# Optimization experiments

Hardware: AMD Instinct MI355X
Metric: run time of the kernel (lower is better)

The kernel has to match this reference:

```python
import jax, jax.numpy as jnp
import numpy as np

EPS = 1e-5
SLOPE = 0.2


def _ico_conv(x, neigh, w, b):
    # x: (B, C, N); neigh: (N, 7) -> gather 1-ring, flatten channel-major, linear
    g = x[:, :, neigh]                          # (B, C, N, 7)
    B, C, N, K = g.shape
    g = g.transpose(0, 2, 1, 3).reshape(B, N, C * K)
    y = jnp.einsum('bnf,of->bno', g, w) + b     # (B, N, out)
    return y.transpose(0, 2, 1)                 # (B, out, N)


def _bn(x, gamma, beta):
    # BatchNorm1d with track_running_stats=False: batch stats over (B, N)
    mean = x.mean(axis=(0, 2), keepdims=True)
    var = x.var(axis=(0, 2), keepdims=True)
    xhat = (x - mean) * jax.lax.rsqrt(var + EPS)
    return xhat * gamma[None, :, None] + beta[None, :, None]


def _lrelu(x):
    return jnp.where(x >= 0, x, SLOPE * x)


def setup_inputs() -> dict:
    key = jax.random.key(0)
    ks = jax.random.split(key, 10)
    B, IN_CH, OUT_CH = 2, 128, 64
    N_DOWN, N_UP, K = 40962, 163842, 7
    inp = {
        'x1': jax.random.normal(ks[0], (B, IN_CH, N_DOWN), jnp.float32),
        'x2': jax.random.normal(ks[1], (B, OUT_CH, N_UP), jnp.float32),
        'up_fc_w': jax.random.normal(ks[2], (OUT_CH, IN_CH), jnp.float32) * 0.05,
        'up_fc_b': jax.random.normal(ks[3], (OUT_CH,), jnp.float32) * 0.05,
        'conv1_w': jax.random.normal(ks[4], (OUT_CH, K * IN_CH), jnp.float32) * 0.05,
        'conv1_b': jax.random.normal(ks[5], (OUT_CH,), jnp.float32) * 0.05,
        'bn1_g': jnp.ones((OUT_CH,), jnp.float32),
        'bn1_b': jnp.zeros((OUT_CH,), jnp.float32),
        'conv2_w': jax.random.normal(ks[6], (OUT_CH, K * OUT_CH), jnp.float32) * 0.05,
        'conv2_b': jax.random.normal(ks[7], (OUT_CH,), jnp.float32) * 0.05,
        'bn2_g': jnp.ones((OUT_CH,), jnp.float32),
        'bn2_b': jnp.zeros((OUT_CH,), jnp.float32),
        'up_neigh': jax.random.randint(ks[8], (N_UP, 2), 0, N_DOWN, jnp.int32),
        'conv_neigh': jax.random.randint(ks[9], (N_UP, K), 0, N_UP, jnp.int32),
        'max_pool_indices': jnp.zeros((1,), jnp.int32),  # unused for up_mode='interp'
    }
    return inp


def reference(x1, x2, up_fc_w, up_fc_b, conv1_w, conv1_b, bn1_g, bn1_b,
              conv2_w, conv2_b, bn2_g, bn2_b, up_neigh, conv_neigh,
              max_pool_indices):
    # --- IcoUpSampleLayer ('interp'): Linear(in->out) then 2-neighbor mean ---
    h = jnp.einsum('bcn,oc->bno', x1, up_fc_w) + up_fc_b   # (B, N_down, out)
    h = h[:, up_neigh].mean(axis=2)                        # (B, N_up, out)
    x1_up = h.transpose(0, 2, 1)                           # (B, out, N_up)
    # --- concat skip along channels ---
    x = jnp.concatenate([x1_up, x2], axis=1)               # (B, in_ch, N_up)
    # --- (conv => BN => LeakyReLU) * 2 ---
    x = _lrelu(_bn(_ico_conv(x, conv_neigh, conv1_w, conv1_b), bn1_g, bn1_b))
    x = _lrelu(_bn(_ico_conv(x, conv_neigh, conv2_w, conv2_b), bn2_g, bn2_b))
    return x
```

## Files before the change

### kernel.cpp

```cpp
#include <hip/hip_runtime.h>
#include <hip/hip_bf16.h>

typedef __hip_bfloat16 bf16;
typedef short bf16x8 __attribute__((ext_vector_type(8)));
typedef float f32x4 __attribute__((ext_vector_type(4)));

#define ND     40962
#define NUP    163842
#define NBATCH 2
#define NTC    2561
#define NT64   2561
#define BN_EPS 1e-5
#define SLOPE  0.2f

#define OFF_W1P   0ull
#define OFF_W2P   114688ull
#define OFF_STATS 172032ull
#define OFF_H     173056ull
#define OFF_P2    (OFF_H + 2622464ull)
#define OFF_XCAT  10659328ull
#define OFF_Y     94546432ull

__device__ __forceinline__ void gload_lds16(const void* g, void* l) {
  __builtin_amdgcn_global_load_lds(
      (const __attribute__((address_space(1))) void*)g,
      (__attribute__((address_space(3))) void*)l, 16, 0, 0);
}

__device__ __forceinline__ float lrelu(float v) { return v >= 0.0f ? v : SLOPE * v; }

__global__ __launch_bounds__(256) void k_permw(const float* __restrict__ w1,
                                               const float* __restrict__ w2,
                                               bf16* __restrict__ w1p, bf16* __restrict__ w2p) {
  int t = blockIdx.x * 256 + threadIdx.x;
  if (t < 64 * 896) {
    int o = t / 896, f = t % 896;
    int kk = f / 128, c = f % 128;
    w1p[t] = __float2bfloat16(w1[o * 896 + c * 7 + kk]);
  } else if (t < 64 * 896 + 64 * 448) {
    int idx = t - 64 * 896;
    int o = idx / 448, f = idx % 448;
    int kk = f / 64, c = f % 64;
    w2p[idx] = __float2bfloat16(w2[o * 448 + c * 7 + kk]);
  }
}

__global__ __launch_bounds__(256) void k_h(const float* __restrict__ x1,
                                           const float* __restrict__ wfc,
                                           const float* __restrict__ bfc,
                                           bf16* __restrict__ h) {
  __shared__ float wl[128 * 64];
  __shared__ float bl[64];
  int tid = threadIdx.x, b = blockIdx.y;
  for (int i = tid; i < 8192; i += 256) { int o = i >> 7, c = i & 127; wl[c * 64 + o] = wfc[i]; }
  if (tid < 64) bl[tid] = bfc[tid];
  __syncthreads();
  int n = blockIdx.x * 256 + tid;
  int nc = n < ND ? n : ND - 1;
  float acc[64];
#pragma unroll
  for (int o = 0; o < 64; ++o) acc[o] = bl[o];
#pragma unroll 4
  for (int c = 0; c < 128; ++c) {
    float xv = x1[((size_t)b * 128 + c) * (size_t)ND + nc];
    const f32x4* wrow = (const f32x4*)(wl + c * 64);
#pragma unroll
    for (int og = 0; og < 16; ++og) {
      f32x4 wv = wrow[og];
      acc[og * 4 + 0] = fmaf(xv, wv[0], acc[og * 4 + 0]);
      acc[og * 4 + 1] = fmaf(xv, wv[1], acc[og * 4 + 1]);
      acc[og * 4 + 2] = fmaf(xv, wv[2], acc[og * 4 + 2]);
      acc[og * 4 + 3] = fmaf(xv, wv[3], acc[og * 4 + 3]);
    }
  }
  if (n < ND) {
    bf16* hp = h + ((size_t)b * ND + n) * 64;
#pragma unroll
    for (int og = 0; og < 8; ++og) {
      union { bf16x8 v; bf16 e[8]; } u;
#pragma unroll
      for (int j = 0; j < 8; ++j) u.e[j] = __float2bfloat16(acc[og * 8 + j]);
      ((bf16x8*)hp)[og] = u.v;
    }
  }
}

__global__ __launch_bounds__(256) void k_xcat(const float* __restrict__ x2,
                                              const bf16* __restrict__ h,
                                              const int* __restrict__ upn,
                                              bf16* __restrict__ xcat) {
  __shared__ float tt[64][65];
  __shared__ int un[64][2];
  int tid = threadIdx.x, b = blockIdx.y;
  int m0 = blockIdx.x * 64;
#pragma unroll
  for (int i = 0; i < 16; ++i) {
    int c = i * 4 + (tid >> 6);
    int ml = tid & 63;
    int m = m0 + ml; if (m >= NUP) m = NUP - 1;
    tt[c][ml] = x2[((size_t)b * 64 + c) * (size_t)NUP + m];
  }
  if (tid < 128) {
    int ml = tid >> 1, w = tid & 1;
    int m = m0 + ml; if (m >= NUP) m = NUP - 1;
    un[ml][w] = upn[(size_t)m * 2 + w];
  }
  __syncthreads();
  int ln = tid >> 2, p = tid & 3;
  int m = m0 + ln;
  if (m >= NUP) return;
  bf16* dst = xcat + ((size_t)b * NUP + m) * 128;
  if (p < 2) {
    int c0 = p * 32;
    const bf16* h0 = h + ((size_t)b * ND + un[ln][0]) * 64 + c0;
    const bf16* h1 = h + ((size_t)b * ND + un[ln][1]) * 64 + c0;
#pragma unroll
    for (int q = 0; q < 4; ++q) {
      union { bf16x8 v; bf16 e[8]; } a, bb, o_;
      a.v = ((const bf16x8*)h0)[q];
      bb.v = ((const bf16x8*)h1)[q];
#pragma unroll
      for (int j = 0; j < 8; ++j)
        o_.e[j] = __float2bfloat16(0.5f * (__bfloat162float(a.e[j]) + __bfloat162float(bb.e[j])));
      ((bf16x8*)(dst + c0))[q] = o_.v;
    }
  } else {
    int c0 = (p - 2) * 32;
#pragma unroll
    for (int q = 0; q < 4; ++q) {
      union { bf16x8 v; bf16 e[8]; } o_;
#pragma unroll
      for (int j = 0; j < 8; ++j) o_.e[j] = __float2bfloat16(tt[c0 + q * 8 + j][ln]);
      ((bf16x8*)(dst + 64 + c0))[q] = o_.v;
    }
  }
}

template <int CIN>
__global__ __launch_bounds__(256, 8) void k_conv(const bf16* __restrict__ x,
                                                 const int* __restrict__ neigh,
                                                 const bf16* __restrict__ wp,
                                                 const float* __restrict__ bias,
                                                 bf16* __restrict__ y,
                                                 float* __restrict__ partials) {
  constexpr int KS    = CIN / 32;
  constexpr int NSTEP = 7 * KS;

  __shared__ bf16 lA[2][2048];
  __shared__ bf16 lW[2][2048];
  __shared__ int nbl[448];

  int tid = threadIdx.x, b = blockIdx.y;
  int n0 = blockIdx.x * 64;
  int wv = tid >> 6, lane = tid & 63;
  int l15 = lane & 15, l4 = lane >> 4;

  for (int j = tid; j < 448; j += 256) {
    int gi = n0 * 7 + j;
    int gmax = NUP * 7 - 1;
    nbl[j] = neigh[gi <= gmax ? gi : gmax];
  }

  f32x4 acc[4];
#pragma unroll
  for (int ot = 0; ot < 4; ++ot) {
    float bv = bias[ot * 16 + l15];
    acc[ot] = (f32x4){bv, bv, bv, bv};
  }

  const bf16* xb = x + (size_t)b * NUP * CIN;
  const int srow = wv * 16 + (lane >> 2);
  const int sg   = ((lane & 3) ^ ((srow >> 1) & 3)) * 8;
  const bf16* wrow_ = wp + (size_t)srow * (7 * CIN) + sg;

  auto STAGE = [&](int buf, int t) {
    int kk = t / KS, ks = t % KS;
    int node = nbl[srow * 7 + kk];
    gload_lds16(xb + (size_t)node * CIN + ks * 32 + sg, &lA[buf][wv * 512]);
    gload_lds16(wrow_ + kk * CIN + ks * 32, &lW[buf][wv * 512]);
  };

  const int r  = wv * 16 + l15;
  const int oa = r * 32 + ((l4 ^ ((l15 >> 1) & 3)) * 8);

  __syncthreads();
  STAGE(0, 0);
  __syncthreads();

  int buf = 0;
#pragma unroll
  for (int t = 0; t < NSTEP; ++t) {
    if (t + 1 < NSTEP) STAGE(buf ^ 1, t + 1);
    bf16x8 a = *(const bf16x8*)(&lA[buf][oa]);
#pragma unroll
    for (int ot = 0; ot < 4; ++ot) {
      int o = ot * 16 + l15;
      bf16x8 bb = *(const bf16x8*)(&lW[buf][o * 32 + ((l4 ^ ((l15 >> 1) & 3)) * 8)]);
      acc[ot] = __builtin_amdgcn_mfma_f32_16x16x32_bf16(a, bb, acc[ot], 0, 0, 0);
    }
    __syncthreads();
    buf ^= 1;
  }

  float* lred = (float*)&lA[0][0];
  float s[4], q[4];
#pragma unroll
  for (int ot = 0; ot < 4; ++ot) { s[ot] = 0.0f; q[ot] = 0.0f; }
  bf16* yb = y + (size_t)b * NUP * 64;
  int nodebase = n0 + wv * 16 + l4 * 4;
#pragma unroll
  for (int i = 0; i < 4; ++i) {
    int node = nodebase + i;
    bool ok = node < NUP;
#pragma unroll
    for (int ot = 0; ot < 4; ++ot) {
      float v = acc[ot][i];
      if (ok) {
        yb[(size_t)node * 64 + ot * 16 + l15] = __float2bfloat16(v);
        s[ot] += v; q[ot] += v * v;
      }
    }
  }
#pragma unroll
  for (int ot = 0; ot < 4; ++ot) {
    s[ot] += __shfl_xor(s[ot], 16); s[ot] += __shfl_xor(s[ot], 32);
    q[ot] += __shfl_xor(q[ot], 16); q[ot] += __shfl_xor(q[ot], 32);
  }
  if (lane < 16) {
#pragma unroll
    for (int ot = 0; ot < 4; ++ot) {
      lred[(wv * 2 + 0) * 64 + ot * 16 + lane] = s[ot];
      lred[(wv * 2 + 1) * 64 + ot * 16 + lane] = q[ot];
    }
  }
  __syncthreads();
  if (tid < 128) {
    int which = tid >> 6, c = tid & 63;
    float p = lred[(0 * 2 + which) * 64 + c] + lred[(1 * 2 + which) * 64 + c] +
              lred[(2 * 2 + which) * 64 + c] + lred[(3 * 2 + which) * 64 + c];
    partials[((size_t)b * gridDim.x + blockIdx.x) * 128 + which * 64 + c] = p;
  }
}

__global__ __launch_bounds__(256) void k_red1(const float* __restrict__ p, int nblk,
                                              float* __restrict__ p2) {
  int g = blockIdx.x * 2 + threadIdx.x / 128;
  int j = threadIdx.x & 127;
  float a = 0.0f;
  for (int r = g; r < nblk; r += 128) a += p[(size_t)r * 128 + j];
  p2[(size_t)g * 128 + j] = a;
}

__global__ __launch_bounds__(128) void k_stats(const float* __restrict__ p2,
                                               const float* __restrict__ g,
                                               const float* __restrict__ be,
                                               float* __restrict__ sc, float* __restrict__ sh) {
  __shared__ double red[128];
  int j = threadIdx.x;
  double a = 0.0;
  for (int r = 0; r < 128; ++r) a += (double)p2[r * 128 + j];
  red[j] = a;
  __syncthreads();
  if (j < 64) {
    double M = (double)NBATCH * (double)NUP;
    double mean = red[j] / M;
    double var = red[64 + j] / M - mean * mean;
    float s = g[j] * (float)(1.0 / sqrt(var + BN_EPS));
    sc[j] = s;
    sh[j] = be[j] - (float)mean * s;
  }
}

__global__ __launch_bounds__(256) void k_bnapply(const bf16* __restrict__ y,
                                                 const float* __restrict__ sc,
                                                 const float* __restrict__ sh,
                                                 bf16* __restrict__ z) {
  __shared__ float ssc[64], ssh[64];
  int tid = threadIdx.x;
  if (tid < 64) { ssc[tid] = sc[tid]; ssh[tid] = sh[tid]; }
  __syncthreads();
  size_t e = ((size_t)blockIdx.x * 256 + tid) * 8;
  if (e >= (size_t)NBATCH * NUP * 64) return;
  int c0 = (int)(e & 63);
  union { bf16x8 v; bf16 el[8]; } in_, o_;
  in_.v = *(const bf16x8*)(y + e);
#pragma unroll
  for (int j = 0; j < 8; ++j) {
    float f = __bfloat162float(in_.el[j]);
    o_.el[j] = __float2bfloat16(lrelu(fmaf(f, ssc[c0 + j], ssh[c0 + j])));
  }
  *(bf16x8*)(z + e) = o_.v;
}

__global__ __launch_bounds__(256) void k_final(const bf16* __restrict__ y,
                                               const float* __restrict__ sc,
                                               const float* __restrict__ sh,
                                               float* __restrict__ out) {
  __shared__ float t[64][65];
  __shared__ float ssc[64], ssh[64];
  int tid = threadIdx.x, b = blockIdx.y;
  int n0 = blockIdx.x * 64;
  if (tid < 64) { ssc[tid] = sc[tid]; ssh[tid] = sh[tid]; }
  __syncthreads();
  int ln = tid >> 2, qc = tid & 3;
  int n = n0 + ln; if (n >= NUP) n = NUP - 1;
  const bf16* yp = y + ((size_t)b * NUP + n) * 64 + qc * 16;
  union { bf16x8 v; bf16 el[8]; } v0, v1;
  v0.v = ((const bf16x8*)yp)[0];
  v1.v = ((const bf16x8*)yp)[1];
#pragma unroll
  for (int j = 0; j < 8; ++j) {
    int c = qc * 16 + j;
    t[ln][c] = lrelu(fmaf(__bfloat162float(v0.el[j]), ssc[c], ssh[c]));
  }
#pragma unroll
  for (int j = 0; j < 8; ++j) {
    int c = qc * 16 + 8 + j;
    t[ln][c] = lrelu(fmaf(__bfloat162float(v1.el[j]), ssc[c], ssh[c]));
  }
  __syncthreads();
  int nl = tid & 63;
  int nn = n0 + nl;
  if (nn >= NUP) return;
#pragma unroll
  for (int i = 0; i < 16; ++i) {
    int c = i * 4 + (tid >> 6);
    out[((size_t)b * 64 + c) * (size_t)NUP + nn] = t[nl][c];
  }
}

extern "C" void kernel_launch(void* const* d_in, const int* in_sizes, int n_in,
                              void* d_out, int out_size, void* d_ws, size_t ws_size,
                              hipStream_t stream) {
  const float* x1      = (const float*)d_in[0];
  const float* x2      = (const float*)d_in[1];
  const float* up_fc_w = (const float*)d_in[2];
  const float* up_fc_b = (const float*)d_in[3];
  const float* conv1_w = (const float*)d_in[4];
  const float* conv1_b = (const float*)d_in[5];
  const float* bn1_g   = (const float*)d_in[6];
  const float* bn1_b   = (const float*)d_in[7];
  const float* conv2_w = (const float*)d_in[8];
  const float* conv2_b = (const float*)d_in[9];
  const float* bn2_g   = (const float*)d_in[10];
  const float* bn2_b   = (const float*)d_in[11];
  const int* up_neigh  = (const int*)d_in[12];
  const int* conv_nei  = (const int*)d_in[13];

  char* ws = (char*)d_ws;
  bf16*  w1p  = (bf16*)(ws + OFF_W1P);
  bf16*  w2p  = (bf16*)(ws + OFF_W2P);
  float* sc   = (float*)(ws + OFF_STATS);
  float* sh   = sc + 64;
  bf16*  h    = (bf16*)(ws + OFF_H);
  float* part = (float*)(ws + OFF_H);
  float* p2   = (float*)(ws + OFF_P2);
  bf16*  xcat = (bf16*)(ws + OFF_XCAT);
  bf16*  z1   = (bf16*)(ws + OFF_XCAT);
  bf16*  y    = (bf16*)(ws + OFF_Y);
  float* out  = (float*)d_out;

  k_permw<<<336, 256, 0, stream>>>(conv1_w, conv2_w, w1p, w2p);
  k_h<<<dim3(161, 2), 256, 0, stream>>>(x1, up_fc_w, up_fc_b, h);
  k_xcat<<<dim3(NT64, 2), 256, 0, stream>>>(x2, h, up_neigh, xcat);
  k_conv<128><<<dim3(NTC, 2), 256, 0, stream>>>(xcat, conv_nei, w1p, conv1_b, y, part);
  k_red1<<<64, 256, 0, stream>>>(part, 2 * NTC, p2);
  k_stats<<<1, 128, 0, stream>>>(p2, bn1_g, bn1_b, sc, sh);
  k_bnapply<<<10241, 256, 0, stream>>>(y, sc, sh, z1);
  k_conv<64><<<dim3(NTC, 2), 256, 0, stream>>>(z1, conv_nei, w2p, conv2_b, y, part);
  k_red1<<<64, 256, 0, stream>>>(part, 2 * NTC, p2);
  k_stats<<<1, 128, 0, stream>>>(p2, bn2_g, bn2_b, sc, sh);
  k_final<<<dim3(NT64, 2), 256, 0, stream>>>(y, sc, sh, out);
}
```

Measured before the change: 353.2 us.

## Fuse BN1+LeakyReLU into conv2 gather and split xcat into separate buffers

Removes the standalone BN-apply pass by applying BN1 scale/shift and LeakyReLU while gathering neighbor rows inside the second convolution. Conv2 now loads A through registers and writes it to LDS instead of using direct global-to-LDS loads. The concatenated xcat buffer is replaced by two separate 64-channel buffers (upsampled h and transposed x2), each written by its own kernel, and conv1 reads from both. This saves a full read/write pass over the intermediate activation. In exchange, conv2 does extra per-element work on every gathered row (7x redundant BN) and its loads become synchronous register loads.

After: 336.5 us. 4.7% less time.

```diff
diff --git a/kernel.cpp b/kernel.cpp
--- a/kernel.cpp
+++ b/kernel.cpp
@@ -9,7 +9,6 @@
 #define NUP    163842
 #define NBATCH 2
 #define NTC    2561
-#define NT64   2561
 #define BN_EPS 1e-5
 #define SLOPE  0.2f
 
@@ -18,7 +17,8 @@
 #define OFF_STATS 172032ull
 #define OFF_H     173056ull
 #define OFF_P2    (OFF_H + 2622464ull)
-#define OFF_XCAT  10659328ull
+#define OFF_HM    10659328ull
+#define OFF_X2T   52602880ull
 #define OFF_Y     94546432ull
 
 __device__ __forceinline__ void gload_lds16(const void* g, void* l) {
@@ -85,12 +85,39 @@
   }
 }
 
-__global__ __launch_bounds__(256) void k_xcat(const float* __restrict__ x2,
-                                              const bf16* __restrict__ h,
-                                              const int* __restrict__ upn,
-                                              bf16* __restrict__ xcat) {
+__global__ __launch_bounds__(256) void k_hm(const bf16* __restrict__ h,
+                                            const int* __restrict__ upn,
+                                            bf16* __restrict__ hm) {
+  __shared__ int un[64][2];
+  int tid = threadIdx.x, b = blockIdx.y;
+  int m0 = blockIdx.x * 64;
+  if (tid < 128) {
+    int ml = tid >> 1, w = tid & 1;
+    int m = m0 + ml; if (m >= NUP) m = NUP - 1;
+    un[ml][w] = upn[(size_t)m * 2 + w];
+  }
+  __syncthreads();
+  int ln = tid >> 2, sg = tid & 3;
+  int m = m0 + ln;
+  if (m >= NUP) return;
+  const bf16* h0 = h + ((size_t)b * ND + un[ln][0]) * 64 + sg * 16;
+  const bf16* h1 = h + ((size_t)b * ND + un[ln][1]) * 64 + sg * 16;
+  bf16* d = hm + ((size_t)b * NUP + m) * 64 + sg * 16;
+#pragma unroll
+  for (int q = 0; q < 2; ++q) {
+    union { bf16x8 v; bf16 e[8]; } a, bb, o_;
+    a.v = ((const bf16x8*)h0)[q];
+    bb.v = ((const bf16x8*)h1)[q];
+#pragma unroll
+    for (int j = 0; j < 8; ++j)
+      o_.e[j] = __float2bfloat16(0.5f * (__bfloat162float(a.e[j]) + __bfloat162float(bb.e[j])));
+    ((bf16x8*)d)[q] = o_.v;
+  }
+}
+
+__global__ __launch_bounds__(256) void k_x2t(const float* __restrict__ x2,
+                                             bf16* __restrict__ x2t) {
   __shared__ float tt[64][65];
-  __shared__ int un[64][2];
   int tid = threadIdx.x, b = blockIdx.y;
   int m0 = blockIdx.x * 64;
 #pragma unroll
@@ -100,52 +127,28 @@
     int m = m0 + ml; if (m >= NUP) m = NUP - 1;
     tt[c][ml] = x2[((size_t)b * 64 + c) * (size_t)NUP + m];
   }
-  if (tid < 128) {
-    int ml = tid >> 1, w = tid & 1;
-    int m = m0 + ml; if (m >= NUP) m = NUP - 1;
-    un[ml][w] = upn[(size_t)m * 2 + w];
-  }
-  __syncthreads();
-  int ln = tid >> 2, p = tid & 3;
+  __syncthreads();
+  int ln = tid >> 2, sg = tid & 3;
   int m = m0 + ln;
   if (m >= NUP) return;
-  bf16* dst = xcat + ((size_t)b * NUP + m) * 128;
-  if (p < 2) {
-    int c0 = p * 32;
-    const bf16* h0 = h + ((size_t)b * ND + un[ln][0]) * 64 + c0;
-    const bf16* h1 = h + ((size_t)b * ND + un[ln][1]) * 64 + c0;
-#pragma unroll
-    for (int q = 0; q < 4; ++q) {
-      union { bf16x8 v; bf16 e[8]; } a, bb, o_;
-      a.v = ((const bf16x8*)h0)[q];
-      bb.v = ((const bf16x8*)h1)[q];
-#pragma unroll
-      for (int j = 0; j < 8; ++j)
-        o_.e[j] = __float2bfloat16(0.5f * (__bfloat162float(a.e[j]) + __bfloat162float(bb.e[j])));
-      ((bf16x8*)(dst + c0))[q] = o_.v;
-    }
-  } else {
-    int c0 = (p - 2) * 32;
-#pragma unroll
-    for (int q = 0; q < 4; ++q) {
-      union { bf16x8 v; bf16 e[8]; } o_;
-#pragma unroll
-      for (int j = 0; j < 8; ++j) o_.e[j] = __float2bfloat16(tt[c0 + q * 8 + j][ln]);
-      ((bf16x8*)(dst + 64 + c0))[q] = o_.v;
-    }
-  }
-}
-
-template <int CIN>
-__global__ __launch_bounds__(256, 8) void k_conv(const bf16* __restrict__ x,
-                                                 const int* __restrict__ neigh,
-                                                 const bf16* __restrict__ wp,
-                                                 const float* __restrict__ bias,
-                                                 bf16* __restrict__ y,
-                                                 float* __restrict__ partials) {
-  constexpr int KS    = CIN / 32;
-  constexpr int NSTEP = 7 * KS;
-
+  bf16* d = x2t + ((size_t)b * NUP + m) * 64 + sg * 16;
+#pragma unroll
+  for (int q = 0; q < 2; ++q) {
+    union { bf16x8 v; bf16 e[8]; } o_;
+#pragma unroll
+    for (int j = 0; j < 8; ++j) o_.e[j] = __float2bfloat16(tt[sg * 16 + q * 8 + j][ln]);
+    ((bf16x8*)d)[q] = o_.v;
+  }
+}
+
+__global__ __launch_bounds__(256, 8) void k_conv1(const bf16* __restrict__ hm,
+                                                  const bf16* __restrict__ x2t,
+                                                  const int* __restrict__ neigh,
+                                                  const bf16* __restrict__ wp,
+                                                  const float* __restrict__ bias,
+                                                  bf16* __restrict__ y,
+                                                  float* __restrict__ partials) {
+  constexpr int NSTEP = 28;
   __shared__ bf16 lA[2][2048];
   __shared__ bf16 lW[2][2048];
   __shared__ int nbl[448];
@@ -168,16 +171,19 @@
     acc[ot] = (f32x4){bv, bv, bv, bv};
   }
 
-  const bf16* xb = x + (size_t)b * NUP * CIN;
+  const bf16* hmb  = hm  + (size_t)b * NUP * 64;
+  const bf16* x2tb = x2t + (size_t)b * NUP * 64;
   const int srow = wv * 16 + (lane >> 2);
   const int sg   = ((lane & 3) ^ ((srow >> 1) & 3)) * 8;
-  const bf16* wrow_ = wp + (size_t)srow * (7 * CIN) + sg;
+  const bf16* wrow_ = wp + (size_t)srow * 896 + sg;
 
   auto STAGE = [&](int buf, int t) {
-    int kk = t / KS, ks = t % KS;
+    int kk = t >> 2, ks = t & 3;
     int node = nbl[srow * 7 + kk];
-    gload_lds16(xb + (size_t)node * CIN + ks * 32 + sg, &lA[buf][wv * 512]);
-    gload_lds16(wrow_ + kk * CIN + ks * 32, &lW[buf][wv * 512]);
+    const bf16* src = (ks < 2) ? (hmb + (size_t)node * 64 + ks * 32)
+                               : (x2tb + (size_t)node * 64 + (ks - 2) * 32);
+    gload_lds16(src + sg, &lA[buf][wv * 512]);
+    gload_lds16(wrow_ + kk * 128 + ks * 32, &lW[buf][wv * 512]);
   };
 
   const int r  = wv * 16 + l15;
@@ -217,6 +223,132 @@
       float v = acc[ot][i];
       if (ok) {
         yb[(size_t)node * 64 + ot * 16 + l15] = __float2bfloat16(v);
+        s[ot] += v; q[ot] += v * v;
+      }
+    }
+  }
+#pragma unroll
+  for (int ot = 0; ot < 4; ++ot) {
+    s[ot] += __shfl_xor(s[ot], 16); s[ot] += __shfl_xor(s[ot], 32);
+    q[ot] += __shfl_xor(q[ot], 16); q[ot] += __shfl_xor(q[ot], 32);
+  }
+  if (lane < 16) {
+#pragma unroll
+    for (int ot = 0; ot < 4; ++ot) {
+      lred[(wv * 2 + 0) * 64 + ot * 16 + lane] = s[ot];
+      lred[(wv * 2 + 1) * 64 + ot * 16 + lane] = q[ot];
+    }
+  }
+  __syncthreads();
+  if (tid < 128) {
+    int which = tid >> 6, c = tid & 63;
+    float p = lred[(0 * 2 + which) * 64 + c] + lred[(1 * 2 + which) * 64 + c] +
+              lred[(2 * 2 + which) * 64 + c] + lred[(3 * 2 + which) * 64 + c];
+    partials[((size_t)b * gridDim.x + blockIdx.x) * 128 + which * 64 + c] = p;
+  }
+}
+
+__global__ __launch_bounds__(256, 8) void k_conv2(const bf16* __restrict__ y,
+                                                  const int* __restrict__ neigh,
+                                                  const bf16* __restrict__ wp,
+                                                  const float* __restrict__ bias,
+                                                  const float* __restrict__ sc,
+                                                  const float* __restrict__ sh,
+                                                  bf16* __restrict__ y2,
+                                                  float* __restrict__ partials) {
+  constexpr int NSTEP = 14;
+  __shared__ bf16 lA[2][2048];
+  __shared__ bf16 lW[2][2048];
+  __shared__ int nbl[448];
+  __shared__ float ssc[64], ssh[64];
+
+  int tid = threadIdx.x, b = blockIdx.y;
+  int n0 = blockIdx.x * 64;
+  int wv = tid >> 6, lane = tid & 63;
+  int l15 = lane & 15, l4 = lane >> 4;
+
+  for (int j = tid; j < 448; j += 256) {
+    int gi = n0 * 7 + j;
+    int gmax = NUP * 7 - 1;
+    nbl[j] = neigh[gi <= gmax ? gi : gmax];
+  }
+  if (tid < 64) { ssc[tid] = sc[tid]; ssh[tid] = sh[tid]; }
+
+  f32x4 acc[4];
+#pragma unroll
+  for (int ot = 0; ot < 4; ++ot) {
+    float bv = bias[ot * 16 + l15];
+    acc[ot] = (f32x4){bv, bv, bv, bv};
+  }
+
+  const bf16* yb = y + (size_t)b * NUP * 64;
+  const int srow = wv * 16 + (lane >> 2);
+  const int seg  = lane & 3;
+  const int slot = (seg ^ ((srow >> 1) & 3)) * 8;
+  const bf16* wrow_ = wp + (size_t)srow * 448 + slot;
+
+  bf16x8 anext;
+  auto STAGE_W = [&](int buf, int t) {
+    int kk = t >> 1, ks = t & 1;
+    gload_lds16(wrow_ + kk * 64 + ks * 32, &lW[buf][wv * 512]);
+  };
+  auto ALOAD = [&](int t) {
+    int kk = t >> 1, ks = t & 1;
+    int node = nbl[srow * 7 + kk];
+    anext = *(const bf16x8*)(yb + (size_t)node * 64 + ks * 32 + seg * 8);
+  };
+  auto BNW = [&](int buf, int t) {
+    int ks = t & 1;
+    union { bf16x8 v; bf16 e[8]; } u, o_;
+    u.v = anext;
+#pragma unroll
+    for (int j = 0; j < 8; ++j) {
+      int c = ks * 32 + seg * 8 + j;
+      float f = __bfloat162float(u.e[j]);
+      o_.e[j] = __float2bfloat16(lrelu(fmaf(f, ssc[c], ssh[c])));
+    }
+    *(bf16x8*)(&lA[buf][srow * 32 + slot]) = o_.v;
+  };
+
+  const int r  = wv * 16 + l15;
+  const int oa = r * 32 + ((l4 ^ ((l15 >> 1) & 3)) * 8);
+
+  __syncthreads();
+  STAGE_W(0, 0); ALOAD(0);
+  __syncthreads();
+  BNW(0, 0);
+
+  int buf = 0;
+#pragma unroll
+  for (int t = 0; t < NSTEP; ++t) {
+    if (t + 1 < NSTEP) { STAGE_W(buf ^ 1, t + 1); ALOAD(t + 1); }
+    bf16x8 a = *(const bf16x8*)(&lA[buf][oa]);
+#pragma unroll
+    for (int ot = 0; ot < 4; ++ot) {
+      int o = ot * 16 + l15;
+      bf16x8 bb = *(const bf16x8*)(&lW[buf][o * 32 + ((l4 ^ ((l15 >> 1) & 3)) * 8)]);
+      acc[ot] = __builtin_amdgcn_mfma_f32_16x16x32_bf16(a, bb, acc[ot], 0, 0, 0);
+    }
+    __syncthreads();
+    if (t + 1 < NSTEP) BNW(buf ^ 1, t + 1);
+    buf ^= 1;
+  }
+
+  float* lred = (float*)&lA[0][0];
+  float s[4], q[4];
+#pragma unroll
+  for (int ot = 0; ot < 4; ++ot) { s[ot] = 0.0f; q[ot] = 0.0f; }
+  bf16* yo = y2 + (size_t)b * NUP * 64;
+  int nodebase = n0 + wv * 16 + l4 * 4;
+#pragma unroll
+  for (int i = 0; i < 4; ++i) {
+    int node = nodebase + i;
+    bool ok = node < NUP;
+#pragma unroll
+    for (int ot = 0; ot < 4; ++ot) {
+      float v = acc[ot][i];
+      if (ok) {
+        yo[(size_t)node * 64 + ot * 16 + l15] = __float2bfloat16(v);
         s[ot] += v; q[ot] += v * v;
       }
     }
@@ -269,27 +401,6 @@
     sc[j] = s;
     sh[j] = be[j] - (float)mean * s;
   }
-}
-
-__global__ __launch_bounds__(256) void k_bnapply(const bf16* __restrict__ y,
-                                                 const float* __restrict__ sc,
-                                                 const float* __restrict__ sh,
-                                                 bf16* __restrict__ z) {
-  __shared__ float ssc[64], ssh[64];
-  int tid = threadIdx.x;
-  if (tid < 64) { ssc[tid] = sc[tid]; ssh[tid] = sh[tid]; }
-  __syncthreads();
-  size_t e = ((size_t)blockIdx.x * 256 + tid) * 8;
-  if (e >= (size_t)NBATCH * NUP * 64) return;
-  int c0 = (int)(e & 63);
-  union { bf16x8 v; bf16 el[8]; } in_, o_;
-  in_.v = *(const bf16x8*)(y + e);
-#pragma unroll
-  for (int j = 0; j < 8; ++j) {
-    float f = __bfloat162float(in_.el[j]);
-    o_.el[j] = __float2bfloat16(lrelu(fmaf(f, ssc[c0 + j], ssh[c0 + j])));
-  }
-  *(bf16x8*)(z + e) = o_.v;
 }
 
 __global__ __launch_bounds__(256) void k_final(const bf16* __restrict__ y,
@@ -355,20 +466,21 @@
   bf16*  h    = (bf16*)(ws + OFF_H);
   float* part = (float*)(ws + OFF_H);
   float* p2   = (float*)(ws + OFF_P2);
-  bf16*  xcat = (bf16*)(ws + OFF_XCAT);
-  bf16*  z1   = (bf16*)(ws + OFF_XCAT);
+  bf16*  hm   = (bf16*)(ws + OFF_HM);
+  bf16*  y2   = (bf16*)(ws + OFF_HM);
+  bf16*  x2t  = (bf16*)(ws + OFF_X2T);
   bf16*  y    = (bf16*)(ws + OFF_Y);
   float* out  = (float*)d_out;
 
   k_permw<<<336, 256, 0, stream>>>(conv1_w, conv2_w, w1p, w2p);
   k_h<<<dim3(161, 2), 256, 0, stream>>>(x1, up_fc_w, up_fc_b, h);
-  k_xcat<<<dim3(NT64, 2), 256, 0, stream>>>(x2, h, up_neigh, xcat);
-  k_conv<128><<<dim3(NTC, 2), 256, 0, stream>>>(xcat, conv_nei, w1p, conv1_b, y, part);
+  k_hm<<<dim3(NTC, 2), 256, 0, stream>>>(h, up_neigh, hm);
+  k_x2t<<<dim3(NTC, 2), 256, 0, stream>>>(x2, x2t);
+  k_conv1<<<dim3(NTC, 2), 256, 0, stream>>>(hm, x2t, conv_nei, w1p, conv1_b, y, part);
   k_red1<<<64, 256, 0, stream>>>(part, 2 * NTC, p2);
   k_stats<<<1, 128, 0, stream>>>(p2, bn1_g, bn1_b, sc, sh);
-  k_bnapply<<<10241, 256, 0, stream>>>(y, sc, sh, z1);
-  k_conv<64><<<dim3(NTC, 2), 256, 0, stream>>>(z1, conv_nei, w2p, conv2_b, y, part);
+  k_conv2<<<dim3(NTC, 2), 256, 0, stream>>>(y, conv_nei, w2p, conv2_b, sc, sh, y2, part);
   k_red1<<<64, 256, 0, stream>>>(part, 2 * NTC, p2);
   k_stats<<<1, 128, 0, stream>>>(p2, bn2_g, bn2_b, sc, sh);
-  k_final<<<dim3(NT64, 2), 256, 0, stream>>>(y, sc, sh, out);
-}
+  k_final<<<dim3(NTC, 2), 256, 0, stream>>>(y2, sc, sh, out);
+}
```
